# Performance work log

Hardware: AMD Instinct MI355X
Metric: run time of the kernel (lower is better)

Reference implementation:

```python
import jax, jax.numpy as jnp
import numpy as np

D = 1024          # label_size / in_features
V = 100000        # vocab size
SHORTLIST = 10000 # cutoffs[0]
# tail clusters: (proj_dim, cluster_size) per div_value=2 schedule
TAILS = [(512, 10000), (256, 20000), (128, 40000), (64, 20000)]


def setup_inputs() -> dict:
    key = jax.random.key(0)
    ks = jax.random.split(key, 11)
    s = jnp.float32(0.02)
    inp = {
        "feature": jax.random.normal(ks[0], (D,), jnp.float32),
        "targets": jax.random.randint(ks[1], (4096,), 0, V),
        "head_w": jax.random.normal(ks[2], (SHORTLIST + len(TAILS), D), jnp.float32) * s,
    }
    for i, (h, c) in enumerate(TAILS):
        inp[f"t{i}p"] = jax.random.normal(ks[3 + 2 * i], (h, D), jnp.float32) * s
        inp[f"t{i}w"] = jax.random.normal(ks[4 + 2 * i], (c, h), jnp.float32) * s
    return inp


def reference(feature, targets, head_w, t0p, t0w, t1p, t1w, t2p, t2w, t3p, t3w):
    # head logits: [SHORTLIST + n_clusters]
    head_lp = jax.nn.log_softmax(head_w @ feature)
    parts = [head_lp[:SHORTLIST]]
    tails = [(t0p, t0w), (t1p, t1w), (t2p, t2w), (t3p, t3w)]
    for i, (p, w) in enumerate(tails):
        # two-stage low-rank projection: [h] then cluster logits [c]
        cl_lp = jax.nn.log_softmax(w @ (p @ feature)) + head_lp[SHORTLIST + i]
        parts.append(cl_lp)
    logprob = jnp.concatenate(parts)  # [V] full-vocab log-probabilities
    return -jnp.mean(logprob[targets])
```

## Files before the change

### kernel.cpp

```cpp
#include <hip/hip_runtime.h>
#include <math.h>

#define NHEAD     10004
#define OFF_HEAD  0
#define OFF_H0    10004
#define OFF_C0    10964
#define OFF_C1    20964
#define OFF_C2    40964
#define OFF_C3    80964
#define OFF_P     100964

#define B_C0   5002
#define B_C1   7502
#define B_C2   10002
#define B_C3   12502
#define NUNITS 13127

__device__ __forceinline__ float wave_sum(float v) {
  v += __shfl_xor(v, 32, 64);
  v += __shfl_xor(v, 16, 64);
  v += __shfl_xor(v, 8, 64);
  v += __shfl_xor(v, 4, 64);
  v += __shfl_xor(v, 2, 64);
  v += __shfl_xor(v, 1, 64);
  return v;
}

__device__ __forceinline__ float dot4(float4 a, float4 c) {
  return a.x * c.x + a.y * c.y + a.z * c.z + a.w * c.w;
}

__global__ __launch_bounds__(256) void proj_kernel(
    const float* __restrict__ feat,
    const float* __restrict__ p0, const float* __restrict__ p1,
    const float* __restrict__ p2, const float* __restrict__ p3,
    float* __restrict__ ws) {
  __shared__ __align__(16) float sf[1024];
  ((float4*)sf)[threadIdx.x] = ((const float4*)feat)[threadIdx.x];
  __syncthreads();
  const float4* sf4 = (const float4*)sf;
  const int lane = threadIdx.x & 63;
  const int pr = blockIdx.x * 4 + (threadIdx.x >> 6);
  const float* src;
  if (pr < 512)      src = p0 + (size_t)pr * 1024;
  else if (pr < 768) src = p1 + (size_t)(pr - 512) * 1024;
  else if (pr < 896) src = p2 + (size_t)(pr - 768) * 1024;
  else               src = p3 + (size_t)(pr - 896) * 1024;
  const float4* src4 = (const float4*)src;
  float4 ld[4];
#pragma unroll
  for (int j = 0; j < 4; ++j) ld[j] = src4[lane + j * 64];
  float acc = 0.f;
#pragma unroll
  for (int j = 0; j < 4; ++j) acc += dot4(ld[j], sf4[lane + j * 64]);
  acc = wave_sum(acc);
  if (lane == 0) ws[NHEAD + pr] = acc;
}

__device__ __forceinline__ void process_unit(
    int u, int lane, const float* sh,
    const float* __restrict__ head_w, const float* __restrict__ w0,
    const float* __restrict__ w1, const float* __restrict__ w2,
    const float* __restrict__ w3, float* __restrict__ ws) {
  float esum = 0.f;
  if (u < B_C0) {
    const float4* sf4 = (const float4*)sh;
    const int r0 = u * 2;
    const float4* w4 = (const float4*)head_w + (size_t)r0 * 256;
    float4 ld[8];
#pragma unroll
    for (int j = 0; j < 4; ++j) ld[j] = w4[lane + j * 64];
#pragma unroll
    for (int j = 0; j < 4; ++j) ld[4 + j] = w4[256 + lane + j * 64];
    float a0 = 0.f, a1 = 0.f;
#pragma unroll
    for (int j = 0; j < 4; ++j) {
      a0 += dot4(ld[j], sf4[lane + j * 64]);
      a1 += dot4(ld[4 + j], sf4[lane + j * 64]);
    }
    a0 = wave_sum(a0); a1 = wave_sum(a1);
    if (lane == 0) { ws[OFF_HEAD + r0] = a0; ws[OFF_HEAD + r0 + 1] = a1; }
    esum = expf(a0) + expf(a1);
  } else if (u < B_C1) {
    const float4* h4 = (const float4*)(sh + 1024);
    const float4 cv0 = h4[lane], cv1 = h4[lane + 64];
    const int r0 = (u - B_C0) * 4;
    const float4* w4 = (const float4*)w0 + (size_t)r0 * 128;
    float4 ld[8];
#pragma unroll
    for (int k = 0; k < 4; ++k) {
      ld[2 * k]     = w4[k * 128 + lane];
      ld[2 * k + 1] = w4[k * 128 + lane + 64];
    }
    float acc[4];
#pragma unroll
    for (int k = 0; k < 4; ++k)
      acc[k] = dot4(ld[2 * k], cv0) + dot4(ld[2 * k + 1], cv1);
#pragma unroll
    for (int k = 0; k < 4; ++k) {
      float a = wave_sum(acc[k]);
      if (lane == 0) ws[OFF_C0 + r0 + k] = a;
      esum += expf(a);
    }
  } else if (u < B_C2) {
    const float4 cv = ((const float4*)(sh + 1536))[lane];
    const int r0 = (u - B_C1) * 8;
    float4 ld[8];
#pragma unroll
    for (int k = 0; k < 8; ++k)
      ld[k] = ((const float4*)w1)[(size_t)(r0 + k) * 64 + lane];
    float acc[8];
#pragma unroll
    for (int k = 0; k < 8; ++k) acc[k] = dot4(ld[k], cv);
#pragma unroll
    for (int k = 0; k < 8; ++k) {
      float a = wave_sum(acc[k]);
      if (lane == 0) ws[OFF_C1 + r0 + k] = a;
      esum += expf(a);
    }
  } else if (u < B_C3) {
    const float4 cv = ((const float4*)(sh + 1792))[lane & 31];
    const int r0 = (u - B_C2) * 16;
    float4 ld[8];
#pragma unroll
    for (int p = 0; p < 8; ++p)
      ld[p] = ((const float4*)w2)[(size_t)(r0 + 2 * p) * 32 + lane];
#pragma unroll
    for (int p = 0; p < 8; ++p) {
      float a = dot4(ld[p], cv);
      a += __shfl_xor(a, 1, 64);
      a += __shfl_xor(a, 2, 64);
      a += __shfl_xor(a, 4, 64);
      a += __shfl_xor(a, 8, 64);
      a += __shfl_xor(a, 16, 64);
      if ((lane & 31) == 0) ws[OFF_C2 + r0 + 2 * p + (lane >> 5)] = a;
      esum += expf(a);
    }
    esum += __shfl_xor(esum, 32, 64);
  } else {
    const float4 cv = ((const float4*)(sh + 1920))[lane & 15];
    const int r0 = (u - B_C3) * 32;
    float4 ld[8];
#pragma unroll
    for (int p = 0; p < 8; ++p)
      ld[p] = ((const float4*)w3)[(size_t)(r0 + 4 * p) * 16 + lane];
#pragma unroll
    for (int p = 0; p < 8; ++p) {
      float a = dot4(ld[p], cv);
      a += __shfl_xor(a, 1, 64);
      a += __shfl_xor(a, 2, 64);
      a += __shfl_xor(a, 4, 64);
      a += __shfl_xor(a, 8, 64);
      if ((lane & 15) == 0) ws[OFF_C3 + r0 + 4 * p + (lane >> 4)] = a;
      esum += expf(a);
    }
    esum += __shfl_xor(esum, 16, 64);
    esum += __shfl_xor(esum, 32, 64);
  }
  if (lane == 0) ws[OFF_P + u] = esum;
}

__global__ __launch_bounds__(256, 4) void main_kernel(
    const float* __restrict__ feat, const float* __restrict__ head_w,
    const float* __restrict__ w0, const float* __restrict__ w1,
    const float* __restrict__ w2, const float* __restrict__ w3,
    float* __restrict__ ws) {
  __shared__ __align__(16) float sh[1984];
  const int t = threadIdx.x;
  ((float4*)sh)[t] = ((const float4*)feat)[t];
  if (t < 240) ((float4*)(sh + 1024))[t] = ((const float4*)(ws + OFF_H0))[t];
  __syncthreads();
  const int lane = t & 63;
  const int u = blockIdx.x * 4 + (t >> 6);
  if (u < NUNITS)
    process_unit(u, lane, sh, head_w, w0, w1, w2, w3, ws);
}

__global__ __launch_bounds__(1024) void finalize_kernel(
    const int* __restrict__ targets, float* __restrict__ ws,
    float* __restrict__ out) {
  const int tid = threadIdx.x;
  const int wv = tid >> 6, lane = tid & 63;
  float tv[4]; int sg[4];
#pragma unroll
  for (int it = 0; it < 4; ++it) {
    int tgt = targets[tid + it * 1024];
    int addr = tgt + ((tgt >= 10000) ? 964 : 0);
    tv[it] = ws[addr];
    sg[it] = (tgt >= 10000) + (tgt >= 20000) + (tgt >= 40000) + (tgt >= 80000);
  }
  float a0 = 0.f, a1 = 0.f, a2 = 0.f, a3 = 0.f, a4 = 0.f;
#pragma unroll
  for (int it = 0; it < 13; ++it) {
    int i = tid + it * 1024;
    if (i < NUNITS) {
      float v = ws[OFF_P + i];
      if (i < B_C0)      a0 += v;
      else if (i < B_C1) a1 += v;
      else if (i < B_C2) a2 += v;
      else if (i < B_C3) a3 += v;
      else               a4 += v;
    }
  }
  a0 = wave_sum(a0); a1 = wave_sum(a1); a2 = wave_sum(a2);
  a3 = wave_sum(a3); a4 = wave_sum(a4);
  __shared__ float r5[16][5];
  __shared__ float slse[5];
  if (lane == 0) { r5[wv][0] = a0; r5[wv][1] = a1; r5[wv][2] = a2; r5[wv][3] = a3; r5[wv][4] = a4; }
  __syncthreads();
  if (tid < 5) {
    float s = 0.f;
#pragma unroll
    for (int w = 0; w < 16; ++w) s += r5[w][tid];
    slse[tid] = logf(s);
  }
  __syncthreads();
  const float lse0 = slse[0], lse1 = slse[1], lse2 = slse[2], lse3 = slse[3], lse4 = slse[4];
  const float g0 = ws[10000] - lse0, g1 = ws[10001] - lse0;
  const float g2 = ws[10002] - lse0, g3 = ws[10003] - lse0;
  float s = 0.f;
#pragma unroll
  for (int it = 0; it < 4; ++it) {
    int e = sg[it];
    float lseS = (e == 0) ? lse0 : (e == 1) ? lse1 : (e == 2) ? lse2 : (e == 3) ? lse3 : lse4;
    float gS   = (e == 0) ? 0.f  : (e == 1) ? g0   : (e == 2) ? g1   : (e == 3) ? g2   : g3;
    s += tv[it] - lseS + gS;
  }
  s = wave_sum(s);
  if (lane == 0) r5[wv][0] = s;
  __syncthreads();
  if (tid == 0) {
    float tot = 0.f;
#pragma unroll
    for (int w = 0; w < 16; ++w) tot += r5[w][0];
    out[0] = -tot * (1.f / 4096.f);
  }
}

extern "C" void kernel_launch(void* const* d_in, const int* in_sizes, int n_in,
                              void* d_out, int out_size, void* d_ws, size_t ws_size,
                              hipStream_t stream) {
  const float* feat    = (const float*)d_in[0];
  const int*   targets = (const int*)d_in[1];
  const float* head_w  = (const float*)d_in[2];
  const float* t0p = (const float*)d_in[3];
  const float* t0w = (const float*)d_in[4];
  const float* t1p = (const float*)d_in[5];
  const float* t1w = (const float*)d_in[6];
  const float* t2p = (const float*)d_in[7];
  const float* t2w = (const float*)d_in[8];
  const float* t3p = (const float*)d_in[9];
  const float* t3w = (const float*)d_in[10];
  float* ws  = (float*)d_ws;
  float* out = (float*)d_out;

  proj_kernel<<<240, 256, 0, stream>>>(feat, t0p, t1p, t2p, t3p, ws);
  main_kernel<<<3282, 256, 0, stream>>>(feat, head_w, t0w, t1w, t2w, t3w, ws);
  finalize_kernel<<<1, 1024, 0, stream>>>(targets, ws, out);
}
```

Before: 158.5 us.

## Persistent main kernel with double-buffered unit loads and fused last-block finalize

```diff
diff --git a/kernel.cpp b/kernel.cpp
--- a/kernel.cpp
+++ b/kernel.cpp
@@ -9,12 +9,15 @@
 #define OFF_C2    40964
 #define OFF_C3    80964
 #define OFF_P     100964
+#define OFF_CNT   117348
 
 #define B_C0   5002
 #define B_C1   7502
 #define B_C2   10002
 #define B_C3   12502
 #define NUNITS 13127
+#define NBLK   768
+#define STRIDE 3072
 
 __device__ __forceinline__ float wave_sum(float v) {
   v += __shfl_xor(v, 32, 64);
@@ -35,6 +38,7 @@
     const float* __restrict__ p0, const float* __restrict__ p1,
     const float* __restrict__ p2, const float* __restrict__ p3,
     float* __restrict__ ws) {
+  if (blockIdx.x == 0 && threadIdx.x == 0) ((int*)(ws + OFF_CNT))[0] = 0;
   __shared__ __align__(16) float sf[1024];
   ((float4*)sf)[threadIdx.x] = ((const float4*)feat)[threadIdx.x];
   __syncthreads();
@@ -57,21 +61,30 @@
   if (lane == 0) ws[NHEAD + pr] = acc;
 }
 
-__device__ __forceinline__ void process_unit(
-    int u, int lane, const float* sh,
-    const float* __restrict__ head_w, const float* __restrict__ w0,
+__device__ __forceinline__ const float4* unit_base(
+    int u, const float* __restrict__ head_w, const float* __restrict__ w0,
     const float* __restrict__ w1, const float* __restrict__ w2,
-    const float* __restrict__ w3, float* __restrict__ ws) {
-  float esum = 0.f;
+    const float* __restrict__ w3) {
+  const float* p; int v;
+  if (u < B_C0)      { p = head_w; v = u; }
+  else if (u < B_C1) { p = w0; v = u - B_C0; }
+  else if (u < B_C2) { p = w1; v = u - B_C1; }
+  else if (u < B_C3) { p = w2; v = u - B_C2; }
+  else               { p = w3; v = u - B_C3; }
+  return (const float4*)p + (size_t)v * 512;
+}
+
+#define UNIT_LOAD(u, dst) do {                                   \
+    const float4* _bp = unit_base(u, head_w, w0, w1, w2, w3);    \
+    _Pragma("unroll")                                            \
+    for (int _j = 0; _j < 8; ++_j) dst[_j] = _bp[_j * 64 + lane];\
+  } while (0)
+
+__device__ __forceinline__ void unit_compute(
+    int u, int lane, const float* sh, const float4* ld, float* __restrict__ ws) {
+  float esum;
   if (u < B_C0) {
     const float4* sf4 = (const float4*)sh;
-    const int r0 = u * 2;
-    const float4* w4 = (const float4*)head_w + (size_t)r0 * 256;
-    float4 ld[8];
-#pragma unroll
-    for (int j = 0; j < 4; ++j) ld[j] = w4[lane + j * 64];
-#pragma unroll
-    for (int j = 0; j < 4; ++j) ld[4 + j] = w4[256 + lane + j * 64];
     float a0 = 0.f, a1 = 0.f;
 #pragma unroll
     for (int j = 0; j < 4; ++j) {
@@ -79,52 +92,34 @@
       a1 += dot4(ld[4 + j], sf4[lane + j * 64]);
     }
     a0 = wave_sum(a0); a1 = wave_sum(a1);
-    if (lane == 0) { ws[OFF_HEAD + r0] = a0; ws[OFF_HEAD + r0 + 1] = a1; }
+    if (lane == 0) { ws[OFF_HEAD + 2 * u] = a0; ws[OFF_HEAD + 2 * u + 1] = a1; }
     esum = expf(a0) + expf(a1);
   } else if (u < B_C1) {
     const float4* h4 = (const float4*)(sh + 1024);
     const float4 cv0 = h4[lane], cv1 = h4[lane + 64];
     const int r0 = (u - B_C0) * 4;
-    const float4* w4 = (const float4*)w0 + (size_t)r0 * 128;
-    float4 ld[8];
+    esum = 0.f;
 #pragma unroll
     for (int k = 0; k < 4; ++k) {
-      ld[2 * k]     = w4[k * 128 + lane];
-      ld[2 * k + 1] = w4[k * 128 + lane + 64];
-    }
-    float acc[4];
-#pragma unroll
-    for (int k = 0; k < 4; ++k)
-      acc[k] = dot4(ld[2 * k], cv0) + dot4(ld[2 * k + 1], cv1);
-#pragma unroll
-    for (int k = 0; k < 4; ++k) {
-      float a = wave_sum(acc[k]);
+      float a = dot4(ld[2 * k], cv0) + dot4(ld[2 * k + 1], cv1);
+      a = wave_sum(a);
       if (lane == 0) ws[OFF_C0 + r0 + k] = a;
       esum += expf(a);
     }
   } else if (u < B_C2) {
     const float4 cv = ((const float4*)(sh + 1536))[lane];
     const int r0 = (u - B_C1) * 8;
-    float4 ld[8];
-#pragma unroll
-    for (int k = 0; k < 8; ++k)
-      ld[k] = ((const float4*)w1)[(size_t)(r0 + k) * 64 + lane];
-    float acc[8];
-#pragma unroll
-    for (int k = 0; k < 8; ++k) acc[k] = dot4(ld[k], cv);
+    esum = 0.f;
 #pragma unroll
     for (int k = 0; k < 8; ++k) {
-      float a = wave_sum(acc[k]);
+      float a = wave_sum(dot4(ld[k], cv));
       if (lane == 0) ws[OFF_C1 + r0 + k] = a;
       esum += expf(a);
     }
   } else if (u < B_C3) {
     const float4 cv = ((const float4*)(sh + 1792))[lane & 31];
     const int r0 = (u - B_C2) * 16;
-    float4 ld[8];
-#pragma unroll
-    for (int p = 0; p < 8; ++p)
-      ld[p] = ((const float4*)w2)[(size_t)(r0 + 2 * p) * 32 + lane];
+    esum = 0.f;
 #pragma unroll
     for (int p = 0; p < 8; ++p) {
       float a = dot4(ld[p], cv);
@@ -140,10 +135,7 @@
   } else {
     const float4 cv = ((const float4*)(sh + 1920))[lane & 15];
     const int r0 = (u - B_C3) * 32;
-    float4 ld[8];
-#pragma unroll
-    for (int p = 0; p < 8; ++p)
-      ld[p] = ((const float4*)w3)[(size_t)(r0 + 4 * p) * 16 + lane];
+    esum = 0.f;
 #pragma unroll
     for (int p = 0; p < 8; ++p) {
       float a = dot4(ld[p], cv);
@@ -160,39 +152,56 @@
   if (lane == 0) ws[OFF_P + u] = esum;
 }
 
-__global__ __launch_bounds__(256, 4) void main_kernel(
+__global__ __launch_bounds__(256, 3) void main_kernel(
     const float* __restrict__ feat, const float* __restrict__ head_w,
     const float* __restrict__ w0, const float* __restrict__ w1,
     const float* __restrict__ w2, const float* __restrict__ w3,
-    float* __restrict__ ws) {
+    const int* __restrict__ targets, float* __restrict__ ws,
+    float* __restrict__ out) {
   __shared__ __align__(16) float sh[1984];
+  __shared__ float r5[4][5];
+  __shared__ float slse[5];
+  __shared__ int isLast;
   const int t = threadIdx.x;
   ((float4*)sh)[t] = ((const float4*)feat)[t];
   if (t < 240) ((float4*)(sh + 1024))[t] = ((const float4*)(ws + OFF_H0))[t];
   __syncthreads();
   const int lane = t & 63;
-  const int u = blockIdx.x * 4 + (t >> 6);
-  if (u < NUNITS)
-    process_unit(u, lane, sh, head_w, w0, w1, w2, w3, ws);
-}
-
-__global__ __launch_bounds__(1024) void finalize_kernel(
-    const int* __restrict__ targets, float* __restrict__ ws,
-    float* __restrict__ out) {
-  const int tid = threadIdx.x;
-  const int wv = tid >> 6, lane = tid & 63;
-  float tv[4]; int sg[4];
-#pragma unroll
-  for (int it = 0; it < 4; ++it) {
-    int tgt = targets[tid + it * 1024];
-    int addr = tgt + ((tgt >= 10000) ? 964 : 0);
-    tv[it] = ws[addr];
-    sg[it] = (tgt >= 10000) + (tgt >= 20000) + (tgt >= 40000) + (tgt >= 80000);
-  }
+  const int wid = blockIdx.x * 4 + (t >> 6);
+
+  float4 A[8], B[8];
+  const int u0 = wid, u1 = wid + STRIDE, u2 = wid + 2 * STRIDE,
+            u3 = wid + 3 * STRIDE, u4 = wid + 4 * STRIDE;
+  UNIT_LOAD(u0, A);
+  UNIT_LOAD(u1, B);
+  unit_compute(u0, lane, sh, A, ws);
+  UNIT_LOAD(u2, A);
+  unit_compute(u1, lane, sh, B, ws);
+  UNIT_LOAD(u3, B);
+  unit_compute(u2, lane, sh, A, ws);
+  if (u4 < NUNITS) {
+    UNIT_LOAD(u4, A);
+    unit_compute(u3, lane, sh, B, ws);
+    unit_compute(u4, lane, sh, A, ws);
+  } else {
+    unit_compute(u3, lane, sh, B, ws);
+  }
+
+  __threadfence();
+  __syncthreads();
+  if (t == 0) {
+    int old = atomicAdd((int*)(ws + OFF_CNT), 1);
+    isLast = (old == NBLK - 1);
+  }
+  __syncthreads();
+  if (!isLast) return;
+  __threadfence();
+
+  const int wv = t >> 6;
   float a0 = 0.f, a1 = 0.f, a2 = 0.f, a3 = 0.f, a4 = 0.f;
-#pragma unroll
-  for (int it = 0; it < 13; ++it) {
-    int i = tid + it * 1024;
+#pragma unroll 4
+  for (int it = 0; it < 52; ++it) {
+    int i = t + it * 256;
     if (i < NUNITS) {
       float v = ws[OFF_P + i];
       if (i < B_C0)      a0 += v;
@@ -204,37 +213,31 @@
   }
   a0 = wave_sum(a0); a1 = wave_sum(a1); a2 = wave_sum(a2);
   a3 = wave_sum(a3); a4 = wave_sum(a4);
-  __shared__ float r5[16][5];
-  __shared__ float slse[5];
   if (lane == 0) { r5[wv][0] = a0; r5[wv][1] = a1; r5[wv][2] = a2; r5[wv][3] = a3; r5[wv][4] = a4; }
   __syncthreads();
-  if (tid < 5) {
-    float s = 0.f;
-#pragma unroll
-    for (int w = 0; w < 16; ++w) s += r5[w][tid];
-    slse[tid] = logf(s);
+  if (t < 5) {
+    slse[t] = logf(r5[0][t] + r5[1][t] + r5[2][t] + r5[3][t]);
   }
   __syncthreads();
   const float lse0 = slse[0], lse1 = slse[1], lse2 = slse[2], lse3 = slse[3], lse4 = slse[4];
   const float g0 = ws[10000] - lse0, g1 = ws[10001] - lse0;
   const float g2 = ws[10002] - lse0, g3 = ws[10003] - lse0;
   float s = 0.f;
-#pragma unroll
-  for (int it = 0; it < 4; ++it) {
-    int e = sg[it];
+#pragma unroll 4
+  for (int it = 0; it < 16; ++it) {
+    int tgt = targets[t + it * 256];
+    int addr = tgt + ((tgt >= 10000) ? 964 : 0);
+    float lp = ws[addr];
+    int e = (tgt >= 10000) + (tgt >= 20000) + (tgt >= 40000) + (tgt >= 80000);
     float lseS = (e == 0) ? lse0 : (e == 1) ? lse1 : (e == 2) ? lse2 : (e == 3) ? lse3 : lse4;
     float gS   = (e == 0) ? 0.f  : (e == 1) ? g0   : (e == 2) ? g1   : (e == 3) ? g2   : g3;
-    s += tv[it] - lseS + gS;
+    s += lp - lseS + gS;
   }
   s = wave_sum(s);
   if (lane == 0) r5[wv][0] = s;
   __syncthreads();
-  if (tid == 0) {
-    float tot = 0.f;
-#pragma unroll
-    for (int w = 0; w < 16; ++w) tot += r5[w][0];
-    out[0] = -tot * (1.f / 4096.f);
-  }
+  if (t == 0)
+    out[0] = -(r5[0][0] + r5[1][0] + r5[2][0] + r5[3][0]) * (1.f / 4096.f);
 }
 
 extern "C" void kernel_launch(void* const* d_in, const int* in_sizes, int n_in,
@@ -255,6 +258,6 @@
   float* out = (float*)d_out;
 
   proj_kernel<<<240, 256, 0, stream>>>(feat, t0p, t1p, t2p, t3p, ws);
-  main_kernel<<<3282, 256, 0, stream>>>(feat, head_w, t0w, t1w, t2w, t3w, ws);
-  finalize_kernel<<<1, 1024, 0, stream>>>(targets, ws, out);
-}
+  main_kernel<<<NBLK, 256, 0, stream>>>(feat, head_w, t0w, t1w, t2w, t3w,
+                                        targets, ws, out);
+}
```

Measured after the change: 244.2 us. 1.54x slower.

## Fuse finalize into main kernel via last-block atomic counter

Applied to the files above, without the earlier changes.

```diff
diff --git a/kernel.cpp b/kernel.cpp
--- a/kernel.cpp
+++ b/kernel.cpp
@@ -9,12 +9,14 @@
 #define OFF_C2    40964
 #define OFF_C3    80964
 #define OFF_P     100964
+#define OFF_CNT   117348
 
 #define B_C0   5002
 #define B_C1   7502
 #define B_C2   10002
 #define B_C3   12502
 #define NUNITS 13127
+#define NBLK   3282
 
 __device__ __forceinline__ float wave_sum(float v) {
   v += __shfl_xor(v, 32, 64);
@@ -35,6 +37,7 @@
     const float* __restrict__ p0, const float* __restrict__ p1,
     const float* __restrict__ p2, const float* __restrict__ p3,
     float* __restrict__ ws) {
+  if (blockIdx.x == 0 && threadIdx.x == 0) ((int*)(ws + OFF_CNT))[0] = 0;
   __shared__ __align__(16) float sf[1024];
   ((float4*)sf)[threadIdx.x] = ((const float4*)feat)[threadIdx.x];
   __syncthreads();
@@ -164,8 +167,12 @@
     const float* __restrict__ feat, const float* __restrict__ head_w,
     const float* __restrict__ w0, const float* __restrict__ w1,
     const float* __restrict__ w2, const float* __restrict__ w3,
-    float* __restrict__ ws) {
+    const int* __restrict__ targets, float* __restrict__ ws,
+    float* __restrict__ out) {
   __shared__ __align__(16) float sh[1984];
+  __shared__ float r5[4][5];
+  __shared__ float slse[5];
+  __shared__ int isLast;
   const int t = threadIdx.x;
   ((float4*)sh)[t] = ((const float4*)feat)[t];
   if (t < 240) ((float4*)(sh + 1024))[t] = ((const float4*)(ws + OFF_H0))[t];
@@ -174,25 +181,22 @@
   const int u = blockIdx.x * 4 + (t >> 6);
   if (u < NUNITS)
     process_unit(u, lane, sh, head_w, w0, w1, w2, w3, ws);
-}
-
-__global__ __launch_bounds__(1024) void finalize_kernel(
-    const int* __restrict__ targets, float* __restrict__ ws,
-    float* __restrict__ out) {
-  const int tid = threadIdx.x;
-  const int wv = tid >> 6, lane = tid & 63;
-  float tv[4]; int sg[4];
-#pragma unroll
-  for (int it = 0; it < 4; ++it) {
-    int tgt = targets[tid + it * 1024];
-    int addr = tgt + ((tgt >= 10000) ? 964 : 0);
-    tv[it] = ws[addr];
-    sg[it] = (tgt >= 10000) + (tgt >= 20000) + (tgt >= 40000) + (tgt >= 80000);
-  }
+
+  __threadfence();
+  __syncthreads();
+  if (t == 0) {
+    int old = atomicAdd((int*)(ws + OFF_CNT), 1);
+    isLast = (old == NBLK - 1);
+  }
+  __syncthreads();
+  if (!isLast) return;
+  __threadfence();
+
+  const int wv = t >> 6;
   float a0 = 0.f, a1 = 0.f, a2 = 0.f, a3 = 0.f, a4 = 0.f;
-#pragma unroll
-  for (int it = 0; it < 13; ++it) {
-    int i = tid + it * 1024;
+#pragma unroll 4
+  for (int it = 0; it < 52; ++it) {
+    int i = t + it * 256;
     if (i < NUNITS) {
       float v = ws[OFF_P + i];
       if (i < B_C0)      a0 += v;
@@ -204,37 +208,31 @@
   }
   a0 = wave_sum(a0); a1 = wave_sum(a1); a2 = wave_sum(a2);
   a3 = wave_sum(a3); a4 = wave_sum(a4);
-  __shared__ float r5[16][5];
-  __shared__ float slse[5];
   if (lane == 0) { r5[wv][0] = a0; r5[wv][1] = a1; r5[wv][2] = a2; r5[wv][3] = a3; r5[wv][4] = a4; }
   __syncthreads();
-  if (tid < 5) {
-    float s = 0.f;
-#pragma unroll
-    for (int w = 0; w < 16; ++w) s += r5[w][tid];
-    slse[tid] = logf(s);
+  if (t < 5) {
+    slse[t] = logf(r5[0][t] + r5[1][t] + r5[2][t] + r5[3][t]);
   }
   __syncthreads();
   const float lse0 = slse[0], lse1 = slse[1], lse2 = slse[2], lse3 = slse[3], lse4 = slse[4];
   const float g0 = ws[10000] - lse0, g1 = ws[10001] - lse0;
   const float g2 = ws[10002] - lse0, g3 = ws[10003] - lse0;
   float s = 0.f;
-#pragma unroll
-  for (int it = 0; it < 4; ++it) {
-    int e = sg[it];
+#pragma unroll 4
+  for (int it = 0; it < 16; ++it) {
+    int tgt = targets[t + it * 256];
+    int addr = tgt + ((tgt >= 10000) ? 964 : 0);
+    float lp = ws[addr];
+    int e = (tgt >= 10000) + (tgt >= 20000) + (tgt >= 40000) + (tgt >= 80000);
     float lseS = (e == 0) ? lse0 : (e == 1) ? lse1 : (e == 2) ? lse2 : (e == 3) ? lse3 : lse4;
     float gS   = (e == 0) ? 0.f  : (e == 1) ? g0   : (e == 2) ? g1   : (e == 3) ? g2   : g3;
-    s += tv[it] - lseS + gS;
+    s += lp - lseS + gS;
   }
   s = wave_sum(s);
   if (lane == 0) r5[wv][0] = s;
   __syncthreads();
-  if (tid == 0) {
-    float tot = 0.f;
-#pragma unroll
-    for (int w = 0; w < 16; ++w) tot += r5[w][0];
-    out[0] = -tot * (1.f / 4096.f);
-  }
+  if (t == 0)
+    out[0] = -(r5[0][0] + r5[1][0] + r5[2][0] + r5[3][0]) * (1.f / 4096.f);
 }
 
 extern "C" void kernel_launch(void* const* d_in, const int* in_sizes, int n_in,
@@ -255,6 +253,6 @@
   float* out = (float*)d_out;
 
   proj_kernel<<<240, 256, 0, stream>>>(feat, t0p, t1p, t2p, t3p, ws);
-  main_kernel<<<3282, 256, 0, stream>>>(feat, head_w, t0w, t1w, t2w, t3w, ws);
-  finalize_kernel<<<1, 1024, 0, stream>>>(targets, ws, out);
-}
+  main_kernel<<<NBLK, 256, 0, stream>>>(feat, head_w, t0w, t1w, t2w, t3w,
+                                        targets, ws, out);
+}
```

Result: slower. 602.0 us (+279.9%).
